# Performance work log

Hardware: AMD Instinct MI355X
Metric: run time of the kernel (lower is better)

Reference implementation:

```python
import jax, jax.numpy as jnp
import numpy as np

N_NODES = 50000
N_EDGES = 800000
NUM_FEATURES = 128
HIDDEN = 128
NUM_CLASSES = 32


def gcn_conv(x, src, dst, n, W, b):
    loop = jnp.arange(n)
    s = jnp.concatenate([src, loop])
    d = jnp.concatenate([dst, loop])
    deg = jax.ops.segment_sum(jnp.ones_like(d, dtype=x.dtype), d, num_segments=n)
    dinv = jnp.where(deg > 0, jax.lax.rsqrt(deg), 0.0)
    norm = dinv[s] * dinv[d]                      # [E+n]
    h = x @ W                                     # [n, out]
    msg = h[s] * norm[:, None]                    # gather + scale
    out = jax.ops.segment_sum(msg, d, num_segments=n)  # scatter-add
    return out + b


def setup_inputs() -> dict:
    key = jax.random.key(0)
    ks = jax.random.split(key, 9)
    x = jax.random.normal(ks[0], (N_NODES, NUM_FEATURES), dtype=jnp.float32)
    edge_index = jax.random.randint(ks[1], (2, N_EDGES), 0, N_NODES, dtype=jnp.int64)
    sc1 = 1.0 / np.sqrt(NUM_FEATURES)
    sc2 = 1.0 / np.sqrt(HIDDEN)
    W1 = jax.random.uniform(ks[2], (NUM_FEATURES, HIDDEN), jnp.float32, -sc1, sc1)
    b1 = jnp.zeros((HIDDEN,), jnp.float32)
    W2 = jax.random.uniform(ks[3], (HIDDEN, HIDDEN), jnp.float32, -sc2, sc2)
    b2 = jnp.zeros((HIDDEN,), jnp.float32)
    Wfc = jax.random.uniform(ks[4], (HIDDEN, NUM_CLASSES), jnp.float32, -sc2, sc2)
    bfc = jax.random.uniform(ks[5], (NUM_CLASSES,), jnp.float32, -sc2, sc2)
    return {"x": x, "edge_index": edge_index, "W1": W1, "b1": b1,
            "W2": W2, "b2": b2, "Wfc": Wfc, "bfc": bfc}


def reference(x, edge_index, W1, b1, W2, b2, Wfc, bfc):
    n = x.shape[0]
    src, dst = edge_index[0], edge_index[1]
    h = jax.nn.relu(gcn_conv(x, src, dst, n, W1, b1))
    h = jax.nn.relu(gcn_conv(h, src, dst, n, W2, b2))
    # global_mean_pool with batch = zeros -> mean over all nodes, shape [1, HIDDEN]
    pooled = jnp.mean(h, axis=0, keepdims=True)
    return pooled @ Wfc + bfc  # [1, NUM_CLASSES]
```

## Files before the change

kernel.cpp:

```cpp
#include <hip/hip_runtime.h>
#include <stdint.h>

#define FEAT 128
#define ECH 2048
#define CAP 200000

typedef short bf16x8 __attribute__((ext_vector_type(8)));
typedef float f32x4 __attribute__((ext_vector_type(4)));
typedef float f32x2 __attribute__((ext_vector_type(2)));

__device__ __forceinline__ float bfs(unsigned short u) {
    uint32_t t = ((uint32_t)u) << 16;
    return __builtin_bit_cast(float, t);
}
__device__ __forceinline__ unsigned short f2bf(float f) {
    uint32_t u = __builtin_bit_cast(uint32_t, f);
    u += 0x7fffu + ((u >> 16) & 1u);
    return (unsigned short)(u >> 16);
}

__launch_bounds__(256)
__global__ void k_prep(const int* __restrict__ ei,
                       int* __restrict__ dstb, int* __restrict__ srcb,
                       int* __restrict__ bcnt, int* __restrict__ deg,
                       int E, int n, int psz, int NE,
                       const void* W1, const void* W2,
                       const void* b1, const void* b2,
                       const void* Wfc, const void* bfc,
                       unsigned short* Wth1, unsigned short* Wth2,
                       float* b1f, float* b2f, float* Wfcf, float* bfcf) {
    int t = threadIdx.x;

    if ((int)blockIdx.x >= NE) {
        __shared__ int hits;
        int blk = blockIdx.x - NE;
        const void* sampsrc = (blk < 32) ? W1 : (blk < 64 ? W2 : Wfc);
        const uint32_t* samp = (const uint32_t*)sampsrc;
        if (t == 0) hits = 0;
        __syncthreads();
        unsigned ew = (samp[t] >> 7) & 0xFFu;
        unsigned long long bl = __ballot(ew >= 0x60u && ew <= 0x90u);
        if ((t & 63) == 0) atomicAdd(&hits, (int)__popcll(bl));
        __syncthreads();
        int isbf = (2 * hits > 256);

        if (blk < 64) {
            const void* W = (blk < 32) ? W1 : W2;
            unsigned short* th = (blk < 32) ? Wth1 : Wth2;
            int base = (blk & 31) * 512;
            #pragma unroll
            for (int j = 0; j < 2; j++) {
                int idx = base + t * 2 + j;
                int nn = idx >> 7, k = idx & 127;
                int si = k * 128 + nn;
                float f = isbf ? bfs(((const unsigned short*)W)[si])
                               : ((const float*)W)[si];
                th[nn * 128 + k] = f2bf(f);
            }
        } else {
            int i = (blk - 64) * 256 + t;
            if (i >= 4384) return;
            const void* src; float* dst; int off;
            if (i < 128)       { src = b1;  dst = b1f;  off = i; }
            else if (i < 256)  { src = b2;  dst = b2f;  off = i - 128; }
            else if (i < 4352) { src = Wfc; dst = Wfcf; off = i - 256; }
            else               { src = bfc; dst = bfcf; off = i - 4352; }
            dst[off] = isbf ? bfs(((const unsigned short*)src)[off])
                            : ((const float*)src)[off];
        }
        return;
    }

    __shared__ int lflag;
    __shared__ int cnt[8], lofs[8], gbase[8];
    __shared__ int stage_s[ECH];
    __shared__ int stage_d[ECH];
    __shared__ char sb[ECH];
    if (t < 128) {
        int di = blockIdx.x * 128 + t;
        if (di < n) deg[di] = 0;
    }
    if (t == 0) lflag = 0;
    if (t < 8) cnt[t] = 0;
    __syncthreads();
    if (ei[1 + 2 * t] != 0) atomicOr(&lflag, 1);
    __syncthreads();
    int is32 = lflag;

    int base = blockIdx.x * ECH;
    int s[8], d[8], p[8], slot[8];
    #pragma unroll
    for (int j = 0; j < 8; j++) {
        int e = base + j * 256 + t;
        int ss = 0, dd = 0;
        if (e < E) {
            ss = is32 ? ei[e]     : ei[2 * e];
            dd = is32 ? ei[E + e] : ei[2 * E + 2 * e];
            if ((unsigned)ss >= (unsigned)n) ss = 0;
            if ((unsigned)dd >= (unsigned)n) dd = 0;
            int pp = dd / psz;
            if (pp > 7) pp = 7;
            p[j] = pp;
            slot[j] = atomicAdd(&cnt[pp], 1);
        } else p[j] = -1;
        s[j] = ss; d[j] = dd;
    }
    __syncthreads();
    if (t == 0) {
        int acc = 0;
        #pragma unroll
        for (int i = 0; i < 8; i++) { lofs[i] = acc; acc += cnt[i]; }
    }
    __syncthreads();
    if (t < 8) gbase[t] = atomicAdd(&bcnt[t], cnt[t]);
    __syncthreads();
    #pragma unroll
    for (int j = 0; j < 8; j++) {
        if (p[j] >= 0) {
            int pos = lofs[p[j]] + slot[j];
            stage_s[pos] = s[j];
            stage_d[pos] = d[j];
            sb[pos] = (char)p[j];
        }
    }
    __syncthreads();
    int tot = lofs[7] + cnt[7];
    for (int i = t; i < tot; i += 256) {
        int pp = sb[i];
        int off = gbase[pp] + (i - lofs[pp]);
        if (off < CAP) {
            dstb[pp * CAP + off] = stage_d[i];
            srcb[pp * CAP + off] = stage_s[i];
        }
    }
}

__launch_bounds__(256)
__global__ void k_degp(const int* __restrict__ dstb, const int* __restrict__ bcnt,
                       int* __restrict__ deg) {
    int p = blockIdx.x & 7;
    int nb = gridDim.x >> 3;
    int cnt = bcnt[p]; if (cnt > CAP) cnt = CAP;
    const int* db = dstb + p * CAP;
    for (int i = (blockIdx.x >> 3) * 256 + threadIdx.x; i < cnt; i += nb * 256)
        atomicAdd(&deg[db[i]], 1);
}

__global__ void k_bsum(const int* __restrict__ deg, int* __restrict__ bsum,
                       float* __restrict__ dinv, int n) {
    __shared__ int ws[4];
    int t = threadIdx.x, lane = t & 63, w = t >> 6;
    int idx = blockIdx.x * 256 + t;
    int v = (idx < n) ? deg[idx] : 0;
    if (idx < n) dinv[idx] = rsqrtf((float)(v + 1));
    int r = v;
    #pragma unroll
    for (int off = 32; off > 0; off >>= 1) r += __shfl_down(r, off, 64);
    if (lane == 0) ws[w] = r;
    __syncthreads();
    if (t == 0) bsum[blockIdx.x] = ws[0] + ws[1] + ws[2] + ws[3];
}

__launch_bounds__(256)
__global__ void k_bapply2(const int* __restrict__ deg, const int* __restrict__ bsum,
                          int* __restrict__ row_ptr, int* __restrict__ cursor,
                          int n, int nb) {
    __shared__ int wred[4];
    __shared__ int wsum[4];
    __shared__ int boffs;
    int b = blockIdx.x, t = threadIdx.x, lane = t & 63, w = t >> 6;

    int pv = (t < b && t < nb) ? bsum[t] : 0;
    #pragma unroll
    for (int off = 32; off > 0; off >>= 1) pv += __shfl_down(pv, off, 64);
    if (lane == 0) wred[w] = pv;
    __syncthreads();
    if (t == 0) boffs = wred[0] + wred[1] + wred[2] + wred[3];
    __syncthreads();

    int idx = b * 256 + t;
    int v = (idx < n) ? deg[idx] : 0;
    int s = v;
    #pragma unroll
    for (int off = 1; off < 64; off <<= 1) {
        int x = __shfl_up(s, off, 64);
        if (lane >= off) s += x;
    }
    if (lane == 63) wsum[w] = s;
    __syncthreads();
    if (t == 0) {
        int acc = 0;
        #pragma unroll
        for (int i = 0; i < 4; i++) { int x = wsum[i]; wsum[i] = acc; acc += x; }
    }
    __syncthreads();
    int ex = boffs + s - v + wsum[w];
    if (idx < n) {
        row_ptr[idx] = ex;
        cursor[idx]  = ex;
    }
    if (idx == n - 1) row_ptr[n] = ex + v;
}

__launch_bounds__(256)
__global__ void k_scatp(const int* __restrict__ dstb, const int* __restrict__ srcb,
                        const int* __restrict__ bcnt,
                        int* __restrict__ cursor, int* __restrict__ col, int E) {
    int p = blockIdx.x & 7;
    int nb = gridDim.x >> 3;
    int cnt = bcnt[p]; if (cnt > CAP) cnt = CAP;
    const int* db = dstb + p * CAP;
    const int* sb = srcb + p * CAP;
    for (int i = (blockIdx.x >> 3) * 256 + threadIdx.x; i < cnt; i += nb * 256) {
        int pos = atomicAdd(&cursor[db[i]], 1);
        if ((unsigned)pos < (unsigned)E) col[pos] = sb[i];
    }
}

__launch_bounds__(256)
__global__ void k_gemm(const void* __restrict__ X,
                       const unsigned short* __restrict__ Wth,
                       const float* __restrict__ dinv,
                       uint32_t* __restrict__ hs8, int n, int fmt) {
    __shared__ unsigned char lds8[4][16 * 128];
    int wave = threadIdx.x >> 6;
    int l = threadIdx.x & 63;
    int quad = l >> 4;
    int m16 = l & 15;
    int r0 = (blockIdx.x * 4 + wave) * 16;

    int isbf;
    if (fmt != 0) isbf = 1;
    else {
        unsigned ew = (((const uint32_t*)X)[l] >> 7) & 0xFFu;
        unsigned long long bl = __ballot(ew >= 0x60u && ew <= 0x90u);
        isbf = ((int)__popcll(bl) * 2 > 64) ? 1 : 0;
    }

    int ra = r0 + m16;
    if (ra > n - 1) ra = n - 1;
    bf16x8 ah[4];
    if (fmt == 2) {
        const uint2* Xq = (const uint2*)X;
        #pragma unroll
        for (int kt = 0; kt < 4; kt++) {
            uint2 v8 = Xq[ra * 16 + kt * 4 + quad];
            f32x2 p0 = __builtin_amdgcn_cvt_pk_f32_fp8((int)v8.x, false);
            f32x2 p1 = __builtin_amdgcn_cvt_pk_f32_fp8((int)v8.x, true);
            f32x2 p2 = __builtin_amdgcn_cvt_pk_f32_fp8((int)v8.y, false);
            f32x2 p3 = __builtin_amdgcn_cvt_pk_f32_fp8((int)v8.y, true);
            bf16x8 h;
            h[0] = (short)f2bf(p0.x); h[1] = (short)f2bf(p0.y);
            h[2] = (short)f2bf(p1.x); h[3] = (short)f2bf(p1.y);
            h[4] = (short)f2bf(p2.x); h[5] = (short)f2bf(p2.y);
            h[6] = (short)f2bf(p3.x); h[7] = (short)f2bf(p3.y);
            ah[kt] = h;
        }
    } else if (isbf) {
        const int4* Xv = (const int4*)X;
        #pragma unroll
        for (int kt = 0; kt < 4; kt++)
            ah[kt] = __builtin_bit_cast(bf16x8, Xv[ra * 16 + kt * 4 + quad]);
    } else {
        const float4* Xf = (const float4*)X;
        #pragma unroll
        for (int kt = 0; kt < 4; kt++) {
            int jj = kt * 4 + quad;
            float4 fa = Xf[ra * 32 + jj * 2];
            float4 fb = Xf[ra * 32 + jj * 2 + 1];
            float v[8] = {fa.x, fa.y, fa.z, fa.w, fb.x, fb.y, fb.z, fb.w};
            bf16x8 h;
            #pragma unroll
            for (int j = 0; j < 8; j++) h[j] = (short)f2bf(v[j]);
            ah[kt] = h;
        }
    }

    float dv[4];
    #pragma unroll
    for (int reg = 0; reg < 4; reg++) {
        int row = r0 + quad * 4 + reg;
        if (row > n - 1) row = n - 1;
        dv[reg] = dinv[row];
    }

    const int4* Wvh = (const int4*)Wth;
    #pragma unroll
    for (int nt = 0; nt < 8; nt++) {
        f32x4 acc = {0.f, 0.f, 0.f, 0.f};
        int brow = (nt * 16 + m16) * 16;
        #pragma unroll
        for (int kt = 0; kt < 4; kt++) {
            bf16x8 bh = __builtin_bit_cast(bf16x8, Wvh[brow + kt * 4 + quad]);
            acc = __builtin_amdgcn_mfma_f32_16x16x32_bf16(ah[kt], bh, acc, 0, 0, 0);
        }
        #pragma unroll
        for (int reg = 0; reg < 4; reg++) {
            float v = acc[reg] * dv[reg];
            int pk = __builtin_amdgcn_cvt_pk_fp8_f32(v, v, 0, false);
            lds8[wave][(quad * 4 + reg) * 128 + nt * 16 + m16] = (unsigned char)(pk & 0xFF);
        }
    }
    __syncthreads();
    const uint32_t* l32 = (const uint32_t*)lds8[wave];
    #pragma unroll
    for (int i = 0; i < 8; i++) {
        int idx = i * 64 + l;
        int row = idx >> 5;
        int grow = r0 + row;
        if (grow < n) hs8[grow * 32 + (idx & 31)] = l32[idx];
    }
}

__launch_bounds__(256)
__global__ void k_agg(const unsigned short* __restrict__ hsv,
                      const int* __restrict__ row_ptr,
                      const int* __restrict__ col, const float* __restrict__ dinv,
                      const float* __restrict__ bias,
                      unsigned short* __restrict__ out8, float* __restrict__ partial,
                      int n, int E) {
    __shared__ float pl[4][128];
    int wave = threadIdx.x >> 6;
    int lane = threadIdx.x & 63;
    int node = blockIdx.x * 4 + wave;
    bool active = (node < n);
    int nd = active ? node : 0;

    f32x2 sf = __builtin_amdgcn_cvt_pk_f32_fp8((int)hsv[nd * 64 + lane], false);
    float a0 = sf.x, a1 = sf.y;

    int e = row_ptr[nd];
    int end = active ? row_ptr[nd + 1] : e;
    if (e < 0) e = 0;
    if (end > E) end = E;

    for (; e + 8 <= end; e += 8) {
        unsigned s0 = (unsigned)col[e],     s1 = (unsigned)col[e + 1];
        unsigned s2 = (unsigned)col[e + 2], s3 = (unsigned)col[e + 3];
        unsigned s4 = (unsigned)col[e + 4], s5 = (unsigned)col[e + 5];
        unsigned s6 = (unsigned)col[e + 6], s7 = (unsigned)col[e + 7];
        if (s0 >= (unsigned)n) s0 = 0;
        if (s1 >= (unsigned)n) s1 = 0;
        if (s2 >= (unsigned)n) s2 = 0;
        if (s3 >= (unsigned)n) s3 = 0;
        if (s4 >= (unsigned)n) s4 = 0;
        if (s5 >= (unsigned)n) s5 = 0;
        if (s6 >= (unsigned)n) s6 = 0;
        if (s7 >= (unsigned)n) s7 = 0;
        int u0 = hsv[s0 * 64 + lane];
        int u1 = hsv[s1 * 64 + lane];
        int u2 = hsv[s2 * 64 + lane];
        int u3 = hsv[s3 * 64 + lane];
        int u4 = hsv[s4 * 64 + lane];
        int u5 = hsv[s5 * 64 + lane];
        int u6 = hsv[s6 * 64 + lane];
        int u7 = hsv[s7 * 64 + lane];
        f32x2 f0 = __builtin_amdgcn_cvt_pk_f32_fp8(u0, false);
        f32x2 f1 = __builtin_amdgcn_cvt_pk_f32_fp8(u1, false);
        f32x2 f2 = __builtin_amdgcn_cvt_pk_f32_fp8(u2, false);
        f32x2 f3 = __builtin_amdgcn_cvt_pk_f32_fp8(u3, false);
        f32x2 f4 = __builtin_amdgcn_cvt_pk_f32_fp8(u4, false);
        f32x2 f5 = __builtin_amdgcn_cvt_pk_f32_fp8(u5, false);
        f32x2 f6 = __builtin_amdgcn_cvt_pk_f32_fp8(u6, false);
        f32x2 f7 = __builtin_amdgcn_cvt_pk_f32_fp8(u7, false);
        a0 += f0.x + f1.x + f2.x + f3.x + f4.x + f5.x + f6.x + f7.x;
        a1 += f0.y + f1.y + f2.y + f3.y + f4.y + f5.y + f6.y + f7.y;
    }
    for (; e < end; ++e) {
        unsigned s0 = (unsigned)col[e];
        if (s0 >= (unsigned)n) s0 = 0;
        f32x2 f = __builtin_amdgcn_cvt_pk_f32_fp8((int)hsv[s0 * 64 + lane], false);
        a0 += f.x;
        a1 += f.y;
    }

    float dv = dinv[nd];
    float2 bu = ((const float2*)bias)[lane];
    float r0 = fmaxf(dv * a0 + bu.x, 0.f);
    float r1 = fmaxf(dv * a1 + bu.y, 0.f);
    if (!active) { r0 = 0.f; r1 = 0.f; }

    if (out8 != nullptr && active) {
        int pk = __builtin_amdgcn_cvt_pk_fp8_f32(r0, r1, 0, false);
        out8[node * 64 + lane] = (unsigned short)(pk & 0xFFFF);
    }
    if (partial != nullptr) {
        pl[wave][2 * lane]     = r0;
        pl[wave][2 * lane + 1] = r1;
        __syncthreads();
        int t = threadIdx.x;
        if (t < 128) {
            float ps = pl[0][t] + pl[1][t] + pl[2][t] + pl[3][t];
            partial[blockIdx.x * 128 + t] = ps;
        }
    }
}

__launch_bounds__(256)
__global__ void k_redfinal(const float* __restrict__ partial, float* __restrict__ pooled,
                           int* __restrict__ done,
                           const float* __restrict__ Wfcf, const float* __restrict__ bfcf,
                           const void* __restrict__ x, void* __restrict__ out,
                           int n, int nbrows, int gblocks) {
    __shared__ float red[8][128];
    int t = threadIdx.x;
    int chunk = (nbrows + gblocks - 1) / gblocks;
    int r0 = blockIdx.x * chunk;
    int r1 = r0 + chunk;
    if (r1 > nbrows) r1 = nbrows;

    float4 acc = {0.f, 0.f, 0.f, 0.f};
    const float4* p4 = (const float4*)partial;
    for (int i = r0 * 32 + t; i < r1 * 32; i += 256) {
        float4 v = p4[i];
        acc.x += v.x; acc.y += v.y; acc.z += v.z; acc.w += v.w;
    }
    int g = t >> 5;
    int fb = (t & 31) * 4;
    red[g][fb]     = acc.x;
    red[g][fb + 1] = acc.y;
    red[g][fb + 2] = acc.z;
    red[g][fb + 3] = acc.w;
    __syncthreads();
    if (t < 128) {
        float s = red[0][t] + red[1][t] + red[2][t] + red[3][t]
                + red[4][t] + red[5][t] + red[6][t] + red[7][t];
        atomicAdd(&pooled[t], s);
    }
    __threadfence();
    __shared__ int lastf;
    if (t == 0) lastf = (atomicAdd(done, 1) == gblocks - 1) ? 1 : 0;
    __syncthreads();
    if (!lastf) return;

    __shared__ int hits;
    __shared__ float pv[128];
    if (t == 0) hits = 0;
    __syncthreads();
    unsigned ew = (((const uint32_t*)x)[t] >> 7) & 0xFFu;
    unsigned long long bl = __ballot(ew >= 0x60u && ew <= 0x90u);
    if ((t & 63) == 0) atomicAdd(&hits, (int)__popcll(bl));
    if (t < 128)
        pv[t] = __hip_atomic_load(&pooled[t], __ATOMIC_RELAXED,
                                  __HIP_MEMORY_SCOPE_AGENT);
    __syncthreads();
    int isbf = (2 * hits > 256);
    if (t < 32) {
        float s = 0.f;
        for (int c = 0; c < 128; ++c) s += pv[c] * Wfcf[c * 32 + t];
        s = s * (1.0f / (float)n) + bfcf[t];
        if (isbf) ((unsigned short*)out)[t] = f2bf(s);
        else      ((float*)out)[t] = s;
    }
}


extern "C" void kernel_launch(void* const* d_in, const int* in_sizes, int n_in,
                              void* d_out, int out_size, void* d_ws, size_t ws_size,
                              hipStream_t stream) {
    const void* x   = d_in[0];
    const int*  ei  = (const int*)d_in[1];
    const void* W1  = d_in[2];
    const void* b1  = d_in[3];
    const void* W2  = d_in[4];
    const void* b2  = d_in[5];
    const void* Wfc = d_in[6];
    const void* bfc = d_in[7];

    const int n = in_sizes[0] / FEAT;
    const int E = in_sizes[1] / 2;
    const int nagg = (n + 3) / 4;
    const int psz  = (n + 7) / 8;
    const int nscan = (n + 255) / 256;
    const int NE   = (E + ECH - 1) / ECH;

    char* ws = (char*)d_ws;
    uint32_t*       hs8     = (uint32_t*)(ws);
    unsigned short* act8    = (unsigned short*)(ws + 12800000);
    float*          partial = (float*)(ws + 25600000);
    int*            col     = (int*)(ws + 38400000);
    int*            dstb    = (int*)(ws + 41600000);
    int*            srcb    = (int*)(ws + 48000000);
    int*            deg     = (int*)(ws + 54400000);
    int*            row_ptr = (int*)(ws + 54600000);
    int*            cursor  = (int*)(ws + 54800016);
    float*          dinv    = (float*)(ws + 55000016);
    unsigned short* Wth1    = (unsigned short*)(ws + 55200016);
    unsigned short* Wth2    = (unsigned short*)(ws + 55232784);
    float*          b1f     = (float*)(ws + 55265552);
    float*          b2f     = (float*)(ws + 55266064);
    float*          Wfcf    = (float*)(ws + 55266576);
    float*          bfcf    = (float*)(ws + 55282960);
    float*          pooled  = (float*)(ws + 55283088);
    int*            bcnt    = (int*)(ws + 55283600);
    int*            done    = (int*)(ws + 55283632);
    int*            bsum    = (int*)(ws + 55283648);

    if (ws_size < 55284448) return;

    hipMemsetAsync(pooled, 0, 1344, stream);

    k_prep<<<NE + 82, 256, 0, stream>>>(ei, dstb, srcb, bcnt, deg, E, n, psz, NE,
                                        W1, W2, b1, b2, Wfc, bfc,
                                        Wth1, Wth2, b1f, b2f, Wfcf, bfcf);
    k_degp<<<512, 256, 0, stream>>>(dstb, bcnt, deg);
    k_bsum<<<nscan, 256, 0, stream>>>(deg, bsum, dinv, n);
    k_bapply2<<<nscan, 256, 0, stream>>>(deg, bsum, row_ptr, cursor, n, nscan);
    k_scatp<<<512, 256, 0, stream>>>(dstb, srcb, bcnt, cursor, col, E);

    int gemm_grid = (n + 63) / 64;
    k_gemm<<<gemm_grid, 256, 0, stream>>>(x, Wth1, dinv, hs8, n, 0);
    k_agg<<<nagg, 256, 0, stream>>>((const unsigned short*)hs8, row_ptr, col, dinv,
                                    b1f, act8, nullptr, n, E);
    k_gemm<<<gemm_grid, 256, 0, stream>>>(act8, Wth2, dinv, hs8, n, 2);
    k_agg<<<nagg, 256, 0, stream>>>((const unsigned short*)hs8, row_ptr, col, dinv,
                                    b2f, nullptr, partial, n, E);
    k_redfinal<<<100, 256, 0, stream>>>(partial, pooled, done, Wfcf, bfcf,
                                        x, d_out, n, nagg, 100);
}
```

Baseline: 295.5 us.

## Fuse degree counting with first GEMM and split aggregation across wave pairs

The degree-count atomics now run in the same launch as the first-layer GEMM, using separate block ranges, so the two overlap and one launch goes away. This is possible because the source-side normalization is moved out of the GEMM: the aggregation now gathers the source node's inverse square-root degree for every edge. Each node's edge list is split between two waves that combine their partial sums through LDS, which should improve parallelism and latency hiding for the irregular gathers. In exchange, aggregation does an extra per-edge gather of the degree scale and an LDS reduction, and fp8 now stores unscaled GEMM outputs, which can change rounding behaviour.

```diff
diff --git a/kernel.cpp b/kernel.cpp
--- a/kernel.cpp
+++ b/kernel.cpp
@@ -4,6 +4,7 @@
 #define FEAT 128
 #define ECH 2048
 #define CAP 200000
+#define DEGB 512
 
 typedef short bf16x8 __attribute__((ext_vector_type(8)));
 typedef float f32x4 __attribute__((ext_vector_type(4)));
@@ -135,99 +136,14 @@
     }
 }
 
-__launch_bounds__(256)
-__global__ void k_degp(const int* __restrict__ dstb, const int* __restrict__ bcnt,
-                       int* __restrict__ deg) {
-    int p = blockIdx.x & 7;
-    int nb = gridDim.x >> 3;
-    int cnt = bcnt[p]; if (cnt > CAP) cnt = CAP;
-    const int* db = dstb + p * CAP;
-    for (int i = (blockIdx.x >> 3) * 256 + threadIdx.x; i < cnt; i += nb * 256)
-        atomicAdd(&deg[db[i]], 1);
-}
-
-__global__ void k_bsum(const int* __restrict__ deg, int* __restrict__ bsum,
-                       float* __restrict__ dinv, int n) {
-    __shared__ int ws[4];
-    int t = threadIdx.x, lane = t & 63, w = t >> 6;
-    int idx = blockIdx.x * 256 + t;
-    int v = (idx < n) ? deg[idx] : 0;
-    if (idx < n) dinv[idx] = rsqrtf((float)(v + 1));
-    int r = v;
-    #pragma unroll
-    for (int off = 32; off > 0; off >>= 1) r += __shfl_down(r, off, 64);
-    if (lane == 0) ws[w] = r;
-    __syncthreads();
-    if (t == 0) bsum[blockIdx.x] = ws[0] + ws[1] + ws[2] + ws[3];
-}
-
-__launch_bounds__(256)
-__global__ void k_bapply2(const int* __restrict__ deg, const int* __restrict__ bsum,
-                          int* __restrict__ row_ptr, int* __restrict__ cursor,
-                          int n, int nb) {
-    __shared__ int wred[4];
-    __shared__ int wsum[4];
-    __shared__ int boffs;
-    int b = blockIdx.x, t = threadIdx.x, lane = t & 63, w = t >> 6;
-
-    int pv = (t < b && t < nb) ? bsum[t] : 0;
-    #pragma unroll
-    for (int off = 32; off > 0; off >>= 1) pv += __shfl_down(pv, off, 64);
-    if (lane == 0) wred[w] = pv;
-    __syncthreads();
-    if (t == 0) boffs = wred[0] + wred[1] + wred[2] + wred[3];
-    __syncthreads();
-
-    int idx = b * 256 + t;
-    int v = (idx < n) ? deg[idx] : 0;
-    int s = v;
-    #pragma unroll
-    for (int off = 1; off < 64; off <<= 1) {
-        int x = __shfl_up(s, off, 64);
-        if (lane >= off) s += x;
-    }
-    if (lane == 63) wsum[w] = s;
-    __syncthreads();
-    if (t == 0) {
-        int acc = 0;
-        #pragma unroll
-        for (int i = 0; i < 4; i++) { int x = wsum[i]; wsum[i] = acc; acc += x; }
-    }
-    __syncthreads();
-    int ex = boffs + s - v + wsum[w];
-    if (idx < n) {
-        row_ptr[idx] = ex;
-        cursor[idx]  = ex;
-    }
-    if (idx == n - 1) row_ptr[n] = ex + v;
-}
-
-__launch_bounds__(256)
-__global__ void k_scatp(const int* __restrict__ dstb, const int* __restrict__ srcb,
-                        const int* __restrict__ bcnt,
-                        int* __restrict__ cursor, int* __restrict__ col, int E) {
-    int p = blockIdx.x & 7;
-    int nb = gridDim.x >> 3;
-    int cnt = bcnt[p]; if (cnt > CAP) cnt = CAP;
-    const int* db = dstb + p * CAP;
-    const int* sb = srcb + p * CAP;
-    for (int i = (blockIdx.x >> 3) * 256 + threadIdx.x; i < cnt; i += nb * 256) {
-        int pos = atomicAdd(&cursor[db[i]], 1);
-        if ((unsigned)pos < (unsigned)E) col[pos] = sb[i];
-    }
-}
-
-__launch_bounds__(256)
-__global__ void k_gemm(const void* __restrict__ X,
-                       const unsigned short* __restrict__ Wth,
-                       const float* __restrict__ dinv,
-                       uint32_t* __restrict__ hs8, int n, int fmt) {
-    __shared__ unsigned char lds8[4][16 * 128];
-    int wave = threadIdx.x >> 6;
-    int l = threadIdx.x & 63;
+__device__ __forceinline__ void gemm_body(const void* __restrict__ X,
+                                          const unsigned short* __restrict__ Wth,
+                                          uint32_t* __restrict__ hs8,
+                                          int n, int fmt, int tile, int l,
+                                          unsigned char* __restrict__ ldsrow) {
     int quad = l >> 4;
     int m16 = l & 15;
-    int r0 = (blockIdx.x * 4 + wave) * 16;
+    int r0 = tile * 16;
 
     int isbf;
     if (fmt != 0) isbf = 1;
@@ -276,14 +192,6 @@
         }
     }
 
-    float dv[4];
-    #pragma unroll
-    for (int reg = 0; reg < 4; reg++) {
-        int row = r0 + quad * 4 + reg;
-        if (row > n - 1) row = n - 1;
-        dv[reg] = dinv[row];
-    }
-
     const int4* Wvh = (const int4*)Wth;
     #pragma unroll
     for (int nt = 0; nt < 8; nt++) {
@@ -296,19 +204,122 @@
         }
         #pragma unroll
         for (int reg = 0; reg < 4; reg++) {
-            float v = acc[reg] * dv[reg];
+            float v = acc[reg];
             int pk = __builtin_amdgcn_cvt_pk_fp8_f32(v, v, 0, false);
-            lds8[wave][(quad * 4 + reg) * 128 + nt * 16 + m16] = (unsigned char)(pk & 0xFF);
-        }
-    }
-    __syncthreads();
-    const uint32_t* l32 = (const uint32_t*)lds8[wave];
+            ldsrow[(quad * 4 + reg) * 128 + nt * 16 + m16] = (unsigned char)(pk & 0xFF);
+        }
+    }
+    __syncthreads();
+    const uint32_t* l32 = (const uint32_t*)ldsrow;
     #pragma unroll
     for (int i = 0; i < 8; i++) {
         int idx = i * 64 + l;
         int row = idx >> 5;
         int grow = r0 + row;
         if (grow < n) hs8[grow * 32 + (idx & 31)] = l32[idx];
+    }
+}
+
+__launch_bounds__(256)
+__global__ void k_dg(const int* __restrict__ dstb, const int* __restrict__ bcnt,
+                     int* __restrict__ deg,
+                     const void* __restrict__ X,
+                     const unsigned short* __restrict__ Wth,
+                     uint32_t* __restrict__ hs8, int n) {
+    __shared__ unsigned char lds8[4][16 * 128];
+    int b = blockIdx.x;
+    if (b < DEGB) {
+        int p = b & 7;
+        int nb = DEGB >> 3;
+        int cnt = bcnt[p]; if (cnt > CAP) cnt = CAP;
+        const int* db = dstb + p * CAP;
+        for (int i = (b >> 3) * 256 + threadIdx.x; i < cnt; i += nb * 256)
+            atomicAdd(&deg[db[i]], 1);
+        return;
+    }
+    int wave = threadIdx.x >> 6;
+    int l = threadIdx.x & 63;
+    gemm_body(X, Wth, hs8, n, 0, (b - DEGB) * 4 + wave, l, lds8[wave]);
+}
+
+__launch_bounds__(256)
+__global__ void k_gemm(const void* __restrict__ X,
+                       const unsigned short* __restrict__ Wth,
+                       uint32_t* __restrict__ hs8, int n, int fmt) {
+    __shared__ unsigned char lds8[4][16 * 128];
+    int wave = threadIdx.x >> 6;
+    int l = threadIdx.x & 63;
+    gemm_body(X, Wth, hs8, n, fmt, blockIdx.x * 4 + wave, l, lds8[wave]);
+}
+
+__global__ void k_bsum(const int* __restrict__ deg, int* __restrict__ bsum,
+                       float* __restrict__ dinv, int n) {
+    __shared__ int ws[4];
+    int t = threadIdx.x, lane = t & 63, w = t >> 6;
+    int idx = blockIdx.x * 256 + t;
+    int v = (idx < n) ? deg[idx] : 0;
+    if (idx < n) dinv[idx] = rsqrtf((float)(v + 1));
+    int r = v;
+    #pragma unroll
+    for (int off = 32; off > 0; off >>= 1) r += __shfl_down(r, off, 64);
+    if (lane == 0) ws[w] = r;
+    __syncthreads();
+    if (t == 0) bsum[blockIdx.x] = ws[0] + ws[1] + ws[2] + ws[3];
+}
+
+__launch_bounds__(256)
+__global__ void k_bapply2(const int* __restrict__ deg, const int* __restrict__ bsum,
+                          int* __restrict__ row_ptr, int* __restrict__ cursor,
+                          int n, int nb) {
+    __shared__ int wred[4];
+    __shared__ int wsum[4];
+    __shared__ int boffs;
+    int b = blockIdx.x, t = threadIdx.x, lane = t & 63, w = t >> 6;
+
+    int pv = (t < b && t < nb) ? bsum[t] : 0;
+    #pragma unroll
+    for (int off = 32; off > 0; off >>= 1) pv += __shfl_down(pv, off, 64);
+    if (lane == 0) wred[w] = pv;
+    __syncthreads();
+    if (t == 0) boffs = wred[0] + wred[1] + wred[2] + wred[3];
+    __syncthreads();
+
+    int idx = b * 256 + t;
+    int v = (idx < n) ? deg[idx] : 0;
+    int s = v;
+    #pragma unroll
+    for (int off = 1; off < 64; off <<= 1) {
+        int x = __shfl_up(s, off, 64);
+        if (lane >= off) s += x;
+    }
+    if (lane == 63) wsum[w] = s;
+    __syncthreads();
+    if (t == 0) {
+        int acc = 0;
+        #pragma unroll
+        for (int i = 0; i < 4; i++) { int x = wsum[i]; wsum[i] = acc; acc += x; }
+    }
+    __syncthreads();
+    int ex = boffs + s - v + wsum[w];
+    if (idx < n) {
+        row_ptr[idx] = ex;
+        cursor[idx]  = ex;
+    }
+    if (idx == n - 1) row_ptr[n] = ex + v;
+}
+
+__launch_bounds__(256)
+__global__ void k_scatp(const int* __restrict__ dstb, const int* __restrict__ srcb,
+                        const int* __restrict__ bcnt,
+                        int* __restrict__ cursor, int* __restrict__ col, int E) {
+    int p = blockIdx.x & 7;
+    int nb = gridDim.x >> 3;
+    int cnt = bcnt[p]; if (cnt > CAP) cnt = CAP;
+    const int* db = dstb + p * CAP;
+    const int* sb = srcb + p * CAP;
+    for (int i = (blockIdx.x >> 3) * 256 + threadIdx.x; i < cnt; i += nb * 256) {
+        int pos = atomicAdd(&cursor[db[i]], 1);
+        if ((unsigned)pos < (unsigned)E) col[pos] = sb[i];
     }
 }
 
@@ -320,21 +331,35 @@
                       unsigned short* __restrict__ out8, float* __restrict__ partial,
                       int n, int E) {
     __shared__ float pl[4][128];
-    int wave = threadIdx.x >> 6;
+    int w = threadIdx.x >> 6;
     int lane = threadIdx.x & 63;
-    int node = blockIdx.x * 4 + wave;
+    int node = blockIdx.x * 2 + (w >> 1);
+    int half = w & 1;
     bool active = (node < n);
     int nd = active ? node : 0;
 
-    f32x2 sf = __builtin_amdgcn_cvt_pk_f32_fp8((int)hsv[nd * 64 + lane], false);
-    float a0 = sf.x, a1 = sf.y;
-
-    int e = row_ptr[nd];
-    int end = active ? row_ptr[nd + 1] : e;
-    if (e < 0) e = 0;
+    int start = row_ptr[nd];
+    int end = active ? row_ptr[nd + 1] : start;
+    if (start < 0) start = 0;
     if (end > E) end = E;
-
-    for (; e + 8 <= end; e += 8) {
+    int len = end - start;
+    if (len < 0) len = 0;
+    int len1 = ((len >> 1) + 7) & ~7;
+    if (len1 > len) len1 = len;
+
+    float a0, a1;
+    int e, hend;
+    if (half == 0) {
+        float dnd = dinv[nd];
+        f32x2 sf = __builtin_amdgcn_cvt_pk_f32_fp8((int)hsv[nd * 64 + lane], false);
+        a0 = dnd * sf.x; a1 = dnd * sf.y;
+        e = start; hend = start + len1;
+    } else {
+        a0 = 0.f; a1 = 0.f;
+        e = start + len1; hend = end;
+    }
+
+    for (; e + 8 <= hend; e += 8) {
         unsigned s0 = (unsigned)col[e],     s1 = (unsigned)col[e + 1];
         unsigned s2 = (unsigned)col[e + 2], s3 = (unsigned)col[e + 3];
         unsigned s4 = (unsigned)col[e + 4], s5 = (unsigned)col[e + 5];
@@ -347,6 +372,8 @@
         if (s5 >= (unsigned)n) s5 = 0;
         if (s6 >= (unsigned)n) s6 = 0;
         if (s7 >= (unsigned)n) s7 = 0;
+        float d0 = dinv[s0], d1 = dinv[s1], d2 = dinv[s2], d3 = dinv[s3];
+        float d4 = dinv[s4], d5 = dinv[s5], d6 = dinv[s6], d7 = dinv[s7];
         int u0 = hsv[s0 * 64 + lane];
         int u1 = hsv[s1 * 64 + lane];
         int u2 = hsv[s2 * 64 + lane];
@@ -363,36 +390,43 @@
         f32x2 f5 = __builtin_amdgcn_cvt_pk_f32_fp8(u5, false);
         f32x2 f6 = __builtin_amdgcn_cvt_pk_f32_fp8(u6, false);
         f32x2 f7 = __builtin_amdgcn_cvt_pk_f32_fp8(u7, false);
-        a0 += f0.x + f1.x + f2.x + f3.x + f4.x + f5.x + f6.x + f7.x;
-        a1 += f0.y + f1.y + f2.y + f3.y + f4.y + f5.y + f6.y + f7.y;
-    }
-    for (; e < end; ++e) {
+        a0 += d0 * f0.x + d1 * f1.x + d2 * f2.x + d3 * f3.x
+            + d4 * f4.x + d5 * f5.x + d6 * f6.x + d7 * f7.x;
+        a1 += d0 * f0.y + d1 * f1.y + d2 * f2.y + d3 * f3.y
+            + d4 * f4.y + d5 * f5.y + d6 * f6.y + d7 * f7.y;
+    }
+    for (; e < hend; ++e) {
         unsigned s0 = (unsigned)col[e];
         if (s0 >= (unsigned)n) s0 = 0;
+        float d0 = dinv[s0];
         f32x2 f = __builtin_amdgcn_cvt_pk_f32_fp8((int)hsv[s0 * 64 + lane], false);
-        a0 += f.x;
-        a1 += f.y;
-    }
-
-    float dv = dinv[nd];
-    float2 bu = ((const float2*)bias)[lane];
-    float r0 = fmaxf(dv * a0 + bu.x, 0.f);
-    float r1 = fmaxf(dv * a1 + bu.y, 0.f);
-    if (!active) { r0 = 0.f; r1 = 0.f; }
-
-    if (out8 != nullptr && active) {
-        int pk = __builtin_amdgcn_cvt_pk_fp8_f32(r0, r1, 0, false);
-        out8[node * 64 + lane] = (unsigned short)(pk & 0xFFFF);
+        a0 += d0 * f.x;
+        a1 += d0 * f.y;
+    }
+
+    pl[w][2 * lane]     = a0;
+    pl[w][2 * lane + 1] = a1;
+    __syncthreads();
+
+    if (half == 0) {
+        float c0 = pl[w][2 * lane]     + pl[w + 1][2 * lane];
+        float c1 = pl[w][2 * lane + 1] + pl[w + 1][2 * lane + 1];
+        float dv = dinv[nd];
+        float2 bu = ((const float2*)bias)[lane];
+        float r0 = fmaxf(dv * c0 + bu.x, 0.f);
+        float r1 = fmaxf(dv * c1 + bu.y, 0.f);
+        if (!active) { r0 = 0.f; r1 = 0.f; }
+        if (out8 != nullptr && active) {
+            int pk = __builtin_amdgcn_cvt_pk_fp8_f32(r0, r1, 0, false);
+            out8[node * 64 + lane] = (unsigned short)(pk & 0xFFFF);
+        }
+        pl[w][2 * lane]     = r0;
+        pl[w][2 * lane + 1] = r1;
     }
     if (partial != nullptr) {
-        pl[wave][2 * lane]     = r0;
-        pl[wave][2 * lane + 1] = r1;
         __syncthreads();
         int t = threadIdx.x;
-        if (t < 128) {
-            float ps = pl[0][t] + pl[1][t] + pl[2][t] + pl[3][t];
-            partial[blockIdx.x * 128 + t] = ps;
-        }
+        if (t < 128) partial[blockIdx.x * 128 + t] = pl[0][t] + pl[2][t];
     }
 }
 
@@ -469,10 +503,11 @@
 
     const int n = in_sizes[0] / FEAT;
     const int E = in_sizes[1] / 2;
-    const int nagg = (n + 3) / 4;
+    const int nagg2 = (n + 1) / 2;
     const int psz  = (n + 7) / 8;
     const int nscan = (n + 255) / 256;
     const int NE   = (E + ECH - 1) / ECH;
+    const int gemm_grid = ((n + 15) / 16 + 3) / 4;
 
     char* ws = (char*)d_ws;
     uint32_t*       hs8     = (uint32_t*)(ws);
@@ -503,18 +538,16 @@
     k_prep<<<NE + 82, 256, 0, stream>>>(ei, dstb, srcb, bcnt, deg, E, n, psz, NE,
                                         W1, W2, b1, b2, Wfc, bfc,
                                         Wth1, Wth2, b1f, b2f, Wfcf, bfcf);
-    k_degp<<<512, 256, 0, stream>>>(dstb, bcnt, deg);
+    k_dg<<<DEGB + gemm_grid, 256, 0, stream>>>(dstb, bcnt, deg, x, Wth1, hs8, n);
     k_bsum<<<nscan, 256, 0, stream>>>(deg, bsum, dinv, n);
     k_bapply2<<<nscan, 256, 0, stream>>>(deg, bsum, row_ptr, cursor, n, nscan);
     k_scatp<<<512, 256, 0, stream>>>(dstb, srcb, bcnt, cursor, col, E);
 
-    int gemm_grid = (n + 63) / 64;
-    k_gemm<<<gemm_grid, 256, 0, stream>>>(x, Wth1, dinv, hs8, n, 0);
-    k_agg<<<nagg, 256, 0, stream>>>((const unsigned short*)hs8, row_ptr, col, dinv,
-                                    b1f, act8, nullptr, n, E);
-    k_gemm<<<gemm_grid, 256, 0, stream>>>(act8, Wth2, dinv, hs8, n, 2);
-    k_agg<<<nagg, 256, 0, stream>>>((const unsigned short*)hs8, row_ptr, col, dinv,
-                                    b2f, nullptr, partial, n, E);
+    k_agg<<<nagg2, 256, 0, stream>>>((const unsigned short*)hs8, row_ptr, col, dinv,
+                                     b1f, act8, nullptr, n, E);
+    k_gemm<<<gemm_grid, 256, 0, stream>>>(act8, Wth2, hs8, n, 2);
+    k_agg<<<nagg2, 256, 0, stream>>>((const unsigned short*)hs8, row_ptr, col, dinv,
+                                     b2f, nullptr, partial, n, E);
     k_redfinal<<<100, 256, 0, stream>>>(partial, pooled, done, Wfcf, bfcf,
-                                        x, d_out, n, nagg, 100);
-}
+                                        x, d_out, n, nagg2, 100);
+}
```

After: 324.8 us. 1.1x slower.
